# Kernel tuning notes

Hardware: AMD Instinct MI355X
Metric: run time of the kernel (lower is better)

Reference implementation:

```python
import jax, jax.numpy as jnp
import numpy as np

MARGIN = 0.4
SCALE = 80.0
NEG_FILL = -1e30  # used instead of -inf for masked logsumexp (keeps grads NaN-free)

N, D, NUM_CLASSES = 8192, 128, 512


def setup_inputs() -> dict:
    key = jax.random.key(0)
    k1, k2 = jax.random.split(key)
    embeds = jax.random.normal(k1, (N, D), dtype=jnp.float32)
    labels = jax.random.randint(k2, (N,), 0, NUM_CLASSES, dtype=jnp.int64)
    return {"embeds": embeds, "labels": labels}


def _masked_lse(terms, mask):
    # stable logsumexp over axis=1 restricted to mask
    t = jnp.where(mask, terms, NEG_FILL)
    m = jnp.max(t, axis=1, keepdims=True)
    return jnp.squeeze(m, 1) + jnp.log(jnp.sum(jnp.exp(t - m), axis=1))


def reference(embeds, labels):
    # L2-normalize embeddings (F.normalize, p=2, dim=1, eps=1e-12)
    norm = jnp.maximum(jnp.linalg.norm(embeds, axis=1, keepdims=True), 1e-12)
    e = embeds / norm
    sim = e @ e.T  # [N, N]

    same = labels[:, None] == labels[None, :]
    eye = jnp.eye(labels.shape[0], dtype=bool)
    pos_mask = same & ~eye          # positives for each anchor (row)
    neg_mask = ~same                # negatives for each anchor

    # alphas are computed under no_grad in the original
    ap_alpha = jax.lax.stop_gradient(jax.nn.relu(1.0 + MARGIN - sim))
    an_alpha = jax.lax.stop_gradient(jax.nn.relu(sim + MARGIN))

    ap_term = -SCALE * ap_alpha * (sim - 1.0 + MARGIN)
    an_term = SCALE * an_alpha * (sim - MARGIN)

    np_cnt = jnp.sum(pos_mask, axis=1)  # positives per anchor
    nn_cnt = jnp.sum(neg_mask, axis=1)  # negatives per anchor
    valid = (np_cnt > 0) & (nn_cnt > 0)

    # All-triplets logsumexp factorizes: LSE over (p,n) pairs of ap_term[p]
    # equals LSE over p + log(num_neg); symmetric for an_term.
    lse_p = _masked_lse(ap_term, pos_mask)
    lse_n = _masked_lse(an_term, neg_mask)
    log_np = jnp.where(valid, jnp.log(np_cnt.astype(sim.dtype)), 0.0)
    log_nn = jnp.where(valid, jnp.log(nn_cnt.astype(sim.dtype)), 0.0)

    loss_i = jax.nn.softplus(lse_p + log_nn + lse_n + log_np)
    loss = jnp.sum(jnp.where(valid, loss_i, 0.0)) / jnp.maximum(
        jnp.sum(valid).astype(sim.dtype), 1.0)
    return loss
```

## Files before the change

kernel.cpp:

```cpp
#include <hip/hip_runtime.h>
#include <hip/hip_bf16.h>

#define NN_ 8192
#define DD_ 128
#define NCLS 512
#define NSPLIT 16
#define JSPLIT (NN_ / NSPLIT)

typedef short bf16x8 __attribute__((ext_vector_type(8)));
typedef float f32x4 __attribute__((ext_vector_type(4)));

union U4 { uint4 u; bf16x8 h; };

#if __has_builtin(__builtin_amdgcn_exp2f)
#define EXP2(x) __builtin_amdgcn_exp2f(x)
#else
#define EXP2(x) __expf((x) * 0.69314718056f)
#endif

#define C1 115.415603f
#define C2 96.9491065f
#define LN2 0.69314718056f

__device__ __forceinline__ unsigned short f2bf(float f) {
    unsigned int u = __float_as_uint(f);
    unsigned int r = (u + 0x7FFFu + ((u >> 16) & 1u)) >> 16;
    return (unsigned short)r;
}


__global__ __launch_bounds__(512) void k_zero(int* __restrict__ hist) {
    hist[threadIdx.x] = 0;
}

__global__ __launch_bounds__(256) void k_hist(const int* __restrict__ labels,
                                              int* __restrict__ hist) {
    int i = blockIdx.x * 256 + threadIdx.x;
    atomicAdd(&hist[labels[i]], 1);
}

__global__ __launch_bounds__(512) void k_scan(const int* __restrict__ hist,
                                              int* __restrict__ start,
                                              int* __restrict__ base) {
    __shared__ int wsum[8];
    int t = threadIdx.x;
    int v = hist[t];
    int x = v;
#pragma unroll
    for (int m = 1; m < 64; m <<= 1) {
        int y = __shfl_up(x, m);
        if ((t & 63) >= m) x += y;
    }
    if ((t & 63) == 63) wsum[t >> 6] = x;
    __syncthreads();
    int w = t >> 6, woff = 0;
#pragma unroll
    for (int k = 0; k < 8; k++)
        if (k < w) woff += wsum[k];
    int excl = woff + x - v;
    start[t] = excl;
    base[t] = excl;
    if (t == 0) start[NCLS] = NN_;
}

__global__ __launch_bounds__(256) void k_scatter(const int* __restrict__ labels,
                                                 int* __restrict__ base,
                                                 int* __restrict__ srcrow,
                                                 int* __restrict__ plab) {
    int row = blockIdx.x * 256 + threadIdx.x;
    int l = labels[row];
    int p = atomicAdd(&base[l], 1);
    srcrow[p] = row;
    plab[p] = l;
}

__global__ __launch_bounds__(256) void k_norm(const float* __restrict__ x,
                                              const int* __restrict__ srcrow,
                                              unsigned short* __restrict__ ebf) {
    int t = threadIdx.x;
    int r16 = t >> 4;
    int g = t & 15;
    int slot = blockIdx.x * 16 + r16;
    int orig = srcrow[slot];
    const float4* xr = (const float4*)(x + (size_t)orig * DD_);
    float4 v0 = xr[g * 2];
    float4 v1 = xr[g * 2 + 1];
    float ss = v0.x * v0.x + v0.y * v0.y + v0.z * v0.z + v0.w * v0.w +
               v1.x * v1.x + v1.y * v1.y + v1.z * v1.z + v1.w * v1.w;
#pragma unroll
    for (int m = 1; m < 16; m <<= 1) ss += __shfl_xor(ss, m);
    float inv = 1.0f / fmaxf(sqrtf(ss), 1e-12f);
    float vs[8] = {v0.x, v0.y, v0.z, v0.w, v1.x, v1.y, v1.z, v1.w};
    unsigned int p[4];
#pragma unroll
    for (int k = 0; k < 4; k++) {
        unsigned short lo = f2bf(vs[2 * k] * inv);
        unsigned short hi = f2bf(vs[2 * k + 1] * inv);
        p[k] = (unsigned int)lo | ((unsigned int)hi << 16);
    }
    uint4 out = {p[0], p[1], p[2], p[3]};
    ((uint4*)ebf)[blockIdx.x * 256 + g * 16 + r16] = out;
}

__global__ __launch_bounds__(512, 4) void k_main(const unsigned short* __restrict__ ebf,
                                                 const int* __restrict__ plab,
                                                 const int* __restrict__ start,
                                                 float* __restrict__ states) {
    const int lane = threadIdx.x & 63;
    const int wave = threadIdx.x >> 6;
    const int quad = lane >> 4;
    const int lcol = lane & 15;
    const int rowbase = blockIdx.y * 128 + wave * 16;
    const int jsplit = blockIdx.x;
    const int j0 = jsplit * JSPLIT;

    const uint4* fb = (const uint4*)ebf;

    U4 afr[4];
#pragma unroll
    for (int kc = 0; kc < 4; kc++) afr[kc].u = fb[(rowbase >> 4) * 256 + kc * 64 + lane];

    int il[4];
#pragma unroll
    for (int r = 0; r < 4; r++) il[r] = plab[rowbase + quad * 4 + r];

    int labmin = __builtin_amdgcn_readfirstlane(plab[rowbase]);
    int labmax = __builtin_amdgcn_readfirstlane(plab[rowbase + 15]);
    int lo = __builtin_amdgcn_readfirstlane(start[labmin]);
    int hi = __builtin_amdgcn_readfirstlane(start[labmax + 1]);

    float S_an[4] = {0.f, 0.f, 0.f, 0.f};
    float m_p[4] = {-1e30f, -1e30f, -1e30f, -1e30f};
    float s_p[4] = {0.f, 0.f, 0.f, 0.f};
    float cnt[4] = {0.f, 0.f, 0.f, 0.f};

    U4 b0[4], b1[4];
#pragma unroll
    for (int kc = 0; kc < 4; kc++) b0[kc].u = fb[(j0 >> 4) * 256 + kc * 64 + lane];
#pragma unroll
    for (int kc = 0; kc < 4; kc++) b1[kc].u = fb[((j0 + 16) >> 4) * 256 + kc * 64 + lane];

    const int NIT = JSPLIT / 32;
    for (int it = 0; it < NIT; ++it) {
        const int jt = j0 + it * 32;
        const int jp = (it + 1 < NIT) ? jt + 32 : j0;

        {
            f32x4 acc = {0.f, 0.f, 0.f, 0.f};
#pragma unroll
            for (int kc = 0; kc < 4; kc++)
                acc = __builtin_amdgcn_mfma_f32_16x16x32_bf16(afr[kc].h, b0[kc].h, acc, 0, 0, 0);
#pragma unroll
            for (int kc = 0; kc < 4; kc++) b0[kc].u = fb[(jp >> 4) * 256 + kc * 64 + lane];
            if (jt < hi && jt + 16 > lo) {
                int jl = plab[jt + lcol];
                int j = jt + lcol;
#pragma unroll
                for (int r = 0; r < 4; r++) {
                    float s = acc[r];
                    int i = rowbase + quad * 4 + r;
                    bool same = (jl == il[r]);
                    float a = fmaxf(s + 0.4f, 0.0f);
                    float e = EXP2(fmaf(a * C1, s - 0.4f, -C2));
                    S_an[r] += same ? 0.0f : e;
                    cnt[r] += same ? 1.0f : 0.0f;
                    if (same && j != i) {
                        float al = fmaxf(1.4f - s, 0.0f) * (-C1);
                        float tp = al * (s - 0.6f);
                        float mn = fmaxf(m_p[r], tp);
                        s_p[r] = s_p[r] * EXP2(m_p[r] - mn) + EXP2(tp - mn);
                        m_p[r] = mn;
                    }
                }
            } else {
#pragma unroll
                for (int r = 0; r < 4; r++) {
                    float s = acc[r];
                    float a = fmaxf(s + 0.4f, 0.0f);
                    S_an[r] += EXP2(fmaf(a * C1, s - 0.4f, -C2));
                }
            }
        }

        {
            f32x4 acc = {0.f, 0.f, 0.f, 0.f};
#pragma unroll
            for (int kc = 0; kc < 4; kc++)
                acc = __builtin_amdgcn_mfma_f32_16x16x32_bf16(afr[kc].h, b1[kc].h, acc, 0, 0, 0);
#pragma unroll
            for (int kc = 0; kc < 4; kc++) b1[kc].u = fb[((jp + 16) >> 4) * 256 + kc * 64 + lane];
            const int jtt = jt + 16;
            if (jtt < hi && jtt + 16 > lo) {
                int jl = plab[jtt + lcol];
                int j = jtt + lcol;
#pragma unroll
                for (int r = 0; r < 4; r++) {
                    float s = acc[r];
                    int i = rowbase + quad * 4 + r;
                    bool same = (jl == il[r]);
                    float a = fmaxf(s + 0.4f, 0.0f);
                    float e = EXP2(fmaf(a * C1, s - 0.4f, -C2));
                    S_an[r] += same ? 0.0f : e;
                    cnt[r] += same ? 1.0f : 0.0f;
                    if (same && j != i) {
                        float al = fmaxf(1.4f - s, 0.0f) * (-C1);
                        float tp = al * (s - 0.6f);
                        float mn = fmaxf(m_p[r], tp);
                        s_p[r] = s_p[r] * EXP2(m_p[r] - mn) + EXP2(tp - mn);
                        m_p[r] = mn;
                    }
                }
            } else {
#pragma unroll
                for (int r = 0; r < 4; r++) {
                    float s = acc[r];
                    float a = fmaxf(s + 0.4f, 0.0f);
                    S_an[r] += EXP2(fmaf(a * C1, s - 0.4f, -C2));
                }
            }
        }
    }

#pragma unroll
    for (int r = 0; r < 4; r++) {
#pragma unroll
        for (int m = 1; m < 16; m <<= 1) {
            S_an[r] += __shfl_xor(S_an[r], m);
            cnt[r] += __shfl_xor(cnt[r], m);
            float m2 = __shfl_xor(m_p[r], m);
            float s2 = __shfl_xor(s_p[r], m);
            float mn = fmaxf(m_p[r], m2);
            s_p[r] = s_p[r] * EXP2(m_p[r] - mn) + s2 * EXP2(m2 - mn);
            m_p[r] = mn;
        }
    }
    if (lcol == 0) {
#pragma unroll
        for (int r = 0; r < 4; r++) {
            int i = rowbase + quad * 4 + r;
            float4 st = {m_p[r], s_p[r], S_an[r], cnt[r]};
            ((float4*)states)[(size_t)i * NSPLIT + jsplit] = st;
        }
    }
}

__global__ __launch_bounds__(256) void k_fin(const float* __restrict__ states,
                                             float* __restrict__ partials) {
    int i = blockIdx.x * 256 + threadIdx.x;
    float m_p = -1e30f, s_p = 0.f, S_an = 0.f, cnt = 0.f;
#pragma unroll
    for (int k = 0; k < NSPLIT; k++) {
        float4 st = ((const float4*)states)[(size_t)i * NSPLIT + k];
        S_an += st.z;
        cnt += st.w;
        float mn = fmaxf(m_p, st.x);
        s_p = s_p * EXP2(m_p - mn) + st.y * EXP2(st.x - mn);
        m_p = mn;
    }
    int np = (int)cnt - 1;
    int nn = NN_ - (int)cnt;
    float loss = 0.0f, v = 0.0f;
    if (np > 0 && nn > 0 && s_p > 0.f && S_an > 0.f) {
        float lse_p = LN2 * m_p + __logf(s_p);
        float lse_n = 67.2f + __logf(S_an);
        float z = lse_p + lse_n + __logf((float)np) + __logf((float)nn);
        loss = fmaxf(z, 0.0f) + log1pf(__expf(-fabsf(z)));
        v = 1.0f;
    }
#pragma unroll
    for (int m = 1; m < 64; m <<= 1) {
        loss += __shfl_xor(loss, m);
        v += __shfl_xor(v, m);
    }
    if ((threadIdx.x & 63) == 0) {
        int w = (blockIdx.x << 2) | (threadIdx.x >> 6);
        partials[w * 2] = loss;
        partials[w * 2 + 1] = v;
    }
}

__global__ void k_div(const float* __restrict__ partials, float* __restrict__ out) {
    int t = threadIdx.x;
    float loss = partials[t * 2] + partials[(t + 64) * 2];
    float v = partials[t * 2 + 1] + partials[(t + 64) * 2 + 1];
#pragma unroll
    for (int m = 1; m < 64; m <<= 1) {
        loss += __shfl_xor(loss, m);
        v += __shfl_xor(v, m);
    }
    if (t == 0) out[0] = loss / fmaxf(v, 1.0f);
}

extern "C" void kernel_launch(void* const* d_in, const int* in_sizes, int n_in,
                              void* d_out, int out_size, void* d_ws, size_t ws_size,
                              hipStream_t stream) {
    const float* embeds = (const float*)d_in[0];
    const int* labels = (const int*)d_in[1];
    float* out = (float*)d_out;

    char* ws = (char*)d_ws;
    unsigned short* ebf = (unsigned short*)ws;
    float* states = (float*)(ws + 2097152);
    float* partials = (float*)(ws + 4194304);
    int* srcrow = (int*)(ws + 4195328);
    int* plab = (int*)(ws + 4228096);
    int* start = (int*)(ws + 4260864);
    int* base = (int*)(ws + 4263168);
    int* hist = (int*)(ws + 4265216);

    k_zero<<<1, NCLS, 0, stream>>>(hist);
    k_hist<<<NN_ / 256, 256, 0, stream>>>(labels, hist);
    k_scan<<<1, NCLS, 0, stream>>>(hist, start, base);
    k_scatter<<<NN_ / 256, 256, 0, stream>>>(labels, base, srcrow, plab);
    k_norm<<<NN_ / 16, 256, 0, stream>>>(embeds, srcrow, ebf);
    k_main<<<dim3(NSPLIT, NN_ / 128), 512, 0, stream>>>(ebf, plab, start, states);
    k_fin<<<NN_ / 256, 256, 0, stream>>>(states, partials);
    k_div<<<1, 64, 0, stream>>>(partials, out);
}
```

Before: 112.0 us.

## Stage shared B tiles in LDS with double buffering across waves

Each of the 8 waves previously loaded the same 32-column B tile straight from global memory into registers. Now the block loads each tile once cooperatively (one uint4 per thread) into a double-buffered shared-memory array, and waves read their fragments from LDS. This removes redundant global and L2 traffic but adds LDS reads and a block-wide barrier every iteration. It may also reduce register pressure from the old b0/b1 prefetch registers.

```diff
diff --git a/kernel.cpp b/kernel.cpp
--- a/kernel.cpp
+++ b/kernel.cpp
@@ -106,8 +106,11 @@
                                                  const int* __restrict__ plab,
                                                  const int* __restrict__ start,
                                                  float* __restrict__ states) {
-    const int lane = threadIdx.x & 63;
-    const int wave = threadIdx.x >> 6;
+    __shared__ uint4 bsh[1024];
+
+    const int tid = threadIdx.x;
+    const int lane = tid & 63;
+    const int wave = tid >> 6;
     const int quad = lane >> 4;
     const int lcol = lane & 15;
     const int rowbase = blockIdx.y * 128 + wave * 16;
@@ -134,27 +137,33 @@
     float s_p[4] = {0.f, 0.f, 0.f, 0.f};
     float cnt[4] = {0.f, 0.f, 0.f, 0.f};
 
-    U4 b0[4], b1[4];
-#pragma unroll
-    for (int kc = 0; kc < 4; kc++) b0[kc].u = fb[(j0 >> 4) * 256 + kc * 64 + lane];
-#pragma unroll
-    for (int kc = 0; kc < 4; kc++) b1[kc].u = fb[((j0 + 16) >> 4) * 256 + kc * 64 + lane];
+    bsh[tid] = fb[(j0 >> 4) * 256 + tid];
+    __syncthreads();
 
     const int NIT = JSPLIT / 32;
     for (int it = 0; it < NIT; ++it) {
+        const int cur = it & 1;
         const int jt = j0 + it * 32;
-        const int jp = (it + 1 < NIT) ? jt + 32 : j0;
-
-        {
+        const bool has = (it + 1 < NIT);
+
+        uint4 stg;
+        if (has) stg = fb[((jt + 32) >> 4) * 256 + tid];
+
+        const int bb = (cur << 9) + lane;
+
+#pragma unroll
+        for (int c = 0; c < 2; c++) {
+            U4 bf[4];
+#pragma unroll
+            for (int kc = 0; kc < 4; kc++) bf[kc].u = bsh[bb + c * 256 + kc * 64];
             f32x4 acc = {0.f, 0.f, 0.f, 0.f};
 #pragma unroll
             for (int kc = 0; kc < 4; kc++)
-                acc = __builtin_amdgcn_mfma_f32_16x16x32_bf16(afr[kc].h, b0[kc].h, acc, 0, 0, 0);
-#pragma unroll
-            for (int kc = 0; kc < 4; kc++) b0[kc].u = fb[(jp >> 4) * 256 + kc * 64 + lane];
-            if (jt < hi && jt + 16 > lo) {
-                int jl = plab[jt + lcol];
-                int j = jt + lcol;
+                acc = __builtin_amdgcn_mfma_f32_16x16x32_bf16(afr[kc].h, bf[kc].h, acc, 0, 0, 0);
+            const int jc = jt + c * 16;
+            if (jc < hi && jc + 16 > lo) {
+                int jl = plab[jc + lcol];
+                int j = jc + lcol;
 #pragma unroll
                 for (int r = 0; r < 4; r++) {
                     float s = acc[r];
@@ -182,43 +191,8 @@
             }
         }
 
-        {
-            f32x4 acc = {0.f, 0.f, 0.f, 0.f};
-#pragma unroll
-            for (int kc = 0; kc < 4; kc++)
-                acc = __builtin_amdgcn_mfma_f32_16x16x32_bf16(afr[kc].h, b1[kc].h, acc, 0, 0, 0);
-#pragma unroll
-            for (int kc = 0; kc < 4; kc++) b1[kc].u = fb[((jp + 16) >> 4) * 256 + kc * 64 + lane];
-            const int jtt = jt + 16;
-            if (jtt < hi && jtt + 16 > lo) {
-                int jl = plab[jtt + lcol];
-                int j = jtt + lcol;
-#pragma unroll
-                for (int r = 0; r < 4; r++) {
-                    float s = acc[r];
-                    int i = rowbase + quad * 4 + r;
-                    bool same = (jl == il[r]);
-                    float a = fmaxf(s + 0.4f, 0.0f);
-                    float e = EXP2(fmaf(a * C1, s - 0.4f, -C2));
-                    S_an[r] += same ? 0.0f : e;
-                    cnt[r] += same ? 1.0f : 0.0f;
-                    if (same && j != i) {
-                        float al = fmaxf(1.4f - s, 0.0f) * (-C1);
-                        float tp = al * (s - 0.6f);
-                        float mn = fmaxf(m_p[r], tp);
-                        s_p[r] = s_p[r] * EXP2(m_p[r] - mn) + EXP2(tp - mn);
-                        m_p[r] = mn;
-                    }
-                }
-            } else {
-#pragma unroll
-                for (int r = 0; r < 4; r++) {
-                    float s = acc[r];
-                    float a = fmaxf(s + 0.4f, 0.0f);
-                    S_an[r] += EXP2(fmaf(a * C1, s - 0.4f, -C2));
-                }
-            }
-        }
+        if (has) bsh[(cur ^ 1) * 512 + tid] = stg;
+        __syncthreads();
     }
 
 #pragma unroll
```

Measured after the change: 105.7 us. 1.06x faster.
